# Optimization experiments

Measured on AMD Instinct MI355X. Metric: run time of the kernel, lower is better.

Reference implementation:

```python
import jax, jax.numpy as jnp
import numpy as np

N = 100000          # nodes
E = 1600000         # random edges (self loops appended in reference)
F_IN = 256          # dataset.num_features
NUM_CLASSES = 7     # dataset.num_classes
H = 2 * NUM_CLASSES # heads = 14
C = NUM_CLASSES     # per-head channels (concat=False)
NEG_SLOPE = 0.2     # GATConv default leaky_relu slope


def setup_inputs() -> dict:
    key = jax.random.key(0)
    ks = jax.random.split(key, 10)
    x = jax.random.normal(ks[0], (N, F_IN), jnp.float32)
    edge_index = jax.random.randint(ks[1], (2, E), 0, N, jnp.int32)
    def glorot(k, shape, fan_in):
        return jax.random.normal(k, shape, jnp.float32) * (1.0 / np.sqrt(fan_in))
    return {
        "x": x,
        "edge_index": edge_index,
        "W1": glorot(ks[2], (F_IN, H * C), F_IN),
        "a_src1": glorot(ks[3], (H, C), C),
        "a_dst1": glorot(ks[4], (H, C), C),
        "b1": jnp.zeros((C,), jnp.float32),
        "W2": glorot(ks[5], (C, H * C), C),
        "a_src2": glorot(ks[6], (H, C), C),
        "a_dst2": glorot(ks[7], (H, C), C),
        "b2": jnp.zeros((C,), jnp.float32),
    }


def gat_conv(x, src, dst, W, a_src, a_dst, b):
    # x: [N, Fin] -> per-head projections [N, H, C]
    xh = (x @ W).reshape(N, H, C)
    # per-node attention logits [N, H]
    al_src = jnp.einsum("nhc,hc->nh", xh, a_src)
    al_dst = jnp.einsum("nhc,hc->nh", xh, a_dst)
    # per-edge logits (message flows src -> dst)
    alpha = jax.nn.leaky_relu(al_src[src] + al_dst[dst], NEG_SLOPE)  # [E', H]
    # segment softmax over incoming edges of each destination node
    amax = jax.ops.segment_max(jax.lax.stop_gradient(alpha), dst, num_segments=N)
    alpha = jnp.exp(alpha - amax[dst])
    denom = jax.ops.segment_sum(alpha, dst, num_segments=N)
    alpha = alpha / denom[dst]
    # weighted messages, then MAX aggregation per destination (aggr='max')
    msg = alpha[:, :, None] * xh[src]                    # [E', H, C]
    out = jax.ops.segment_max(msg, dst, num_segments=N)  # [N, H, C]
    # concat=False -> mean over heads, plus bias
    return out.mean(axis=1) + b                          # [N, C]


def reference(x, edge_index, W1, a_src1, a_dst1, b1, W2, a_src2, a_dst2, b2):
    # GATConv(add_self_loops=True): append self loops so every node has >=1 in-edge
    loops = jnp.arange(N, dtype=edge_index.dtype)
    src = jnp.concatenate([edge_index[0], loops])
    dst = jnp.concatenate([edge_index[1], loops])
    h = gat_conv(x, src, dst, W1, a_src1, a_dst1, b1)
    h = jax.nn.relu(h)
    h = gat_conv(h, src, dst, W2, a_src2, a_dst2, b2)
    return jax.nn.log_softmax(h, axis=1)
```

## Files before the change

kernel.cpp:

```cpp
#include <hip/hip_runtime.h>
#include <math.h>

#define H  14
#define C  7
#define HC 98
#define FIN 256
#define NEG_SLOPE 0.2f
#define LOG2E 1.44269504088896f

#define BSHIFT 9
#define BSIZE  512
#define NBUCK_MAX 256

typedef __attribute__((ext_vector_type(8))) short short8;
typedef __attribute__((ext_vector_type(4))) float floatx4;
typedef _Float16 h2 __attribute__((ext_vector_type(2)));

#define WT_ROWS   112
#define WT_STRIDE 264
#define XA_STRIDE 40
#define VS_STRIDE 99

__device__ __forceinline__ unsigned bf16r(float f) {
    unsigned u = __float_as_uint(f);
    return (u + 0x7FFFu + ((u >> 16) & 1u)) >> 16;
}

__device__ __forceinline__ h2 u2h(unsigned u) { return __builtin_bit_cast(h2, u); }
__device__ __forceinline__ unsigned hpk(float a, float b) {
    h2 v = { (_Float16)a, (_Float16)b };
    return __builtin_bit_cast(unsigned, v);
}
__device__ __forceinline__ float hhi(unsigned w) {
    unsigned short s = (unsigned short)(w >> 16);
    return (float)__builtin_bit_cast(_Float16, s);
}
__device__ __forceinline__ h2 hshfl_max(h2 v, int mask) {
    int u = __builtin_bit_cast(int, v);
    int o = __shfl_xor(u, mask, 64);
    return __builtin_elementwise_max(v, u2h((unsigned)o));
}


__global__ void k_zero(int* __restrict__ p, int n) {
    int i = blockIdx.x * blockDim.x + threadIdx.x;
    if (i < n) p[i] = 0;
}

__global__ __launch_bounds__(256) void k_hist(const int* __restrict__ ei, int E,
                                              int* __restrict__ gcnt, int nb) {
    __shared__ int hist[NBUCK_MAX];
    const int t = threadIdx.x;
    for (int i = t; i < nb; i += 256) hist[i] = 0;
    __syncthreads();
    const int stride = gridDim.x * 256;
    for (int e = blockIdx.x * 256 + t; e < E; e += stride)
        atomicAdd(&hist[ei[E + e] >> BSHIFT], 1);
    __syncthreads();
    for (int i = t; i < nb; i += 256)
        if (hist[i]) atomicAdd(gcnt + i, hist[i]);
}

__global__ __launch_bounds__(1024) void k_bscan(const int* __restrict__ gcnt,
                                                int* __restrict__ boff, int* __restrict__ bcur,
                                                int* __restrict__ row_ptr, int nb, int N) {
    __shared__ int sd[1024];
    int t = threadIdx.x;
    int own = (t < nb) ? gcnt[t] : 0;
    sd[t] = own;
    __syncthreads();
    #pragma unroll
    for (int off = 1; off < 1024; off <<= 1) {
        int v = (t >= off) ? sd[t - off] : 0;
        __syncthreads();
        sd[t] += v;
        __syncthreads();
    }
    if (t < nb) {
        boff[t + 1] = sd[t];
        bcur[t] = sd[t] - own;
        if (t == nb - 1) row_ptr[N] = sd[t];
    }
    if (t == 0) boff[0] = 0;
}

__global__ __launch_bounds__(256) void k_part(const int* __restrict__ ei, int E,
                                              int* __restrict__ bcur, int2* __restrict__ pedge,
                                              int nb) {
    __shared__ int hist[NBUCK_MAX];
    __shared__ int start[NBUCK_MAX];
    const int t = threadIdx.x;
    const int chunk = (E + gridDim.x - 1) / gridDim.x;
    const int c0 = blockIdx.x * chunk;
    const int c1 = min(c0 + chunk, E);
    for (int i = t; i < nb; i += 256) hist[i] = 0;
    __syncthreads();
    for (int e = c0 + t; e < c1; e += 256)
        atomicAdd(&hist[ei[E + e] >> BSHIFT], 1);
    __syncthreads();
    for (int i = t; i < nb; i += 256) {
        int h = hist[i];
        start[i] = h ? atomicAdd(bcur + i, h) : 0;
        hist[i] = 0;
    }
    __syncthreads();
    for (int e = c0 + t; e < c1; e += 256) {
        int s = ei[e], d = ei[E + e];
        int b = d >> BSHIFT;
        int pos = start[b] + atomicAdd(&hist[b], 1);
        pedge[pos] = make_int2(s, d);
    }
}

__global__ __launch_bounds__(512) void k_bcsr(const int2* __restrict__ pedge,
                                              const int* __restrict__ boff,
                                              int* __restrict__ row_ptr, int* __restrict__ col,
                                              int N) {
    __shared__ int cnt[BSIZE];
    __shared__ int sc[BSIZE];
    __shared__ int cur[BSIZE];
    const int b  = blockIdx.x;
    const int t  = threadIdx.x;
    const int e0 = boff[b], e1 = boff[b + 1];
    const int base = b << BSHIFT;
    const int nv = min(BSIZE, N - base);
    cnt[t] = 0;
    __syncthreads();
    for (int e = e0 + t; e < e1; e += 512)
        atomicAdd(&cnt[pedge[e].y - base], 1);
    __syncthreads();
    sc[t] = cnt[t];
    __syncthreads();
    #pragma unroll
    for (int off = 1; off < BSIZE; off <<= 1) {
        int v = (t >= off) ? sc[t - off] : 0;
        __syncthreads();
        sc[t] += v;
        __syncthreads();
    }
    if (t < nv) {
        int excl = sc[t] - cnt[t];
        row_ptr[base + t] = e0 + excl;
        cur[t] = excl;
    }
    __syncthreads();
    for (int e = e0 + t; e < e1; e += 512) {
        int2 r = pedge[e];
        int d = r.y - base;
        int pos = e0 + atomicAdd(&cur[d], 1);
        col[pos] = r.x;
    }
}


__global__ void k_convW(const float* __restrict__ W, unsigned short* __restrict__ WtG) {
    int id = blockIdx.x * blockDim.x + threadIdx.x;
    int n = id >> 8, k = id & 255;
    float v = (n < HC) ? W[k * HC + n] : 0.f;
    WtG[id] = (unsigned short)(__float_as_uint(v) >> 16);
}

__global__ __launch_bounds__(256) void k_proj1_mfma(
    const float* __restrict__ x, const unsigned short* __restrict__ WtG,
    const float* __restrict__ asrc, const float* __restrict__ adst,
    uint4* __restrict__ xpack, float* __restrict__ aldst, int N)
{
    __shared__ unsigned short wt_s[WT_ROWS * WT_STRIDE];
    __shared__ unsigned short xa_s[64 * XA_STRIDE];
    __shared__ float as_s[HC], ad_s[HC];
    float* vals_s = (float*)wt_s;
    const int t  = threadIdx.x;
    const int wv = t >> 6;
    const int l  = t & 63;
    const int ln = l & 15;
    const int qd = l >> 4;
    const int rowBase = blockIdx.x * 64;

    #pragma unroll
    for (int i = 0; i < 14; ++i) {
        int f = i * 256 + t;
        int r = f >> 5, pos = f & 31;
        *(uint4*)(wt_s + r * WT_STRIDE + pos * 8) = ((const uint4*)WtG)[f];
    }
    if (t < HC) { as_s[t] = asrc[t]; ad_s[t] = adst[t]; }

    floatx4 acc[7] = {};

    for (int step = 0; step < 8; ++step) {
        const int k0 = step * 32;
        __syncthreads();
        #pragma unroll
        for (int i = 0; i < 2; ++i) {
            int idx = i * 256 + t;
            int r = idx >> 3, c4 = idx & 7;
            int gr = rowBase + r; if (gr >= N) gr = N - 1;
            float4 v = *(const float4*)(x + (size_t)gr * FIN + k0 + c4 * 4);
            ushort4 u;
            u.x = (unsigned short)(__float_as_uint(v.x) >> 16);
            u.y = (unsigned short)(__float_as_uint(v.y) >> 16);
            u.z = (unsigned short)(__float_as_uint(v.z) >> 16);
            u.w = (unsigned short)(__float_as_uint(v.w) >> 16);
            *(ushort4*)(xa_s + r * XA_STRIDE + c4 * 4) = u;
        }
        __syncthreads();
        short8 a = *(const short8*)(xa_s + ((wv << 4) + ln) * XA_STRIDE + qd * 8);
        #pragma unroll
        for (int ct = 0; ct < 7; ++ct) {
            short8 b = *(const short8*)(wt_s + (ct * 16 + ln) * WT_STRIDE + k0 + qd * 8);
            acc[ct] = __builtin_amdgcn_mfma_f32_16x16x32_bf16(a, b, acc[ct], 0, 0, 0);
        }
    }

    __syncthreads();
    #pragma unroll
    for (int ct = 0; ct < 7; ++ct) {
        int colg = ct * 16 + ln;
        if (colg < HC) {
            #pragma unroll
            for (int r = 0; r < 4; ++r)
                vals_s[((wv << 4) + (qd << 2) + r) * VS_STRIDE + colg] = acc[ct][r];
        }
    }
    __syncthreads();

    for (int p = t; p < 64 * H; p += 256) {
        int nl = p / H, h = p - nl * H;
        int gn = rowBase + nl;
        if (gn >= N) break;
        const float* vp = vals_s + nl * VS_STRIDE + h * C;
        float v[C];
        float s1 = 0.f, s2 = 0.f;
        #pragma unroll
        for (int c2 = 0; c2 < C; ++c2) {
            float f = vp[c2];
            v[c2] = f;
            s1 = fmaf(f, as_s[h * C + c2], s1);
            s2 = fmaf(f, ad_s[h * C + c2], s2);
        }
        uint4 pk;
        pk.x = hpk(v[0], v[1]);
        pk.y = hpk(v[2], v[3]);
        pk.z = hpk(v[4], v[5]);
        pk.w = hpk(v[6], s1 * LOG2E);
        xpack[(size_t)gn * H + h] = pk;
        aldst[(size_t)gn * H + h] = s2 * LOG2E;
    }
}


__global__ __launch_bounds__(256) void k_proj2_pack(
    const float* __restrict__ h1, const float* __restrict__ W,
    const float* __restrict__ asrc, const float* __restrict__ adst,
    uint4* __restrict__ xpack, float* __restrict__ aldst, int N)
{
    __shared__ float Ws[C * HC];
    __shared__ float as_s[HC], ad_s[HC];
    const int t = threadIdx.x;
    for (int i = t; i < C * HC; i += 256) Ws[i] = W[i];
    if (t < HC) { as_s[t] = asrc[t]; ad_s[t] = adst[t]; }
    __syncthreads();
    int n = blockIdx.x * 256 + t;
    if (n >= N) return;
    float xr[C];
    #pragma unroll
    for (int c2 = 0; c2 < C; ++c2) xr[c2] = h1[(size_t)n * C + c2];
    #pragma unroll
    for (int h = 0; h < H; ++h) {
        float v[C], s1 = 0.f, s2 = 0.f;
        #pragma unroll
        for (int c2 = 0; c2 < C; ++c2) {
            float acc = 0.f;
            #pragma unroll
            for (int k = 0; k < C; ++k)
                acc = fmaf(xr[k], Ws[k * HC + h * C + c2], acc);
            v[c2] = acc;
            s1 = fmaf(acc, as_s[h * C + c2], s1);
            s2 = fmaf(acc, ad_s[h * C + c2], s2);
        }
        uint4 pk;
        pk.x = hpk(v[0], v[1]);
        pk.y = hpk(v[2], v[3]);
        pk.z = hpk(v[4], v[5]);
        pk.w = hpk(v[6], s1 * LOG2E);
        xpack[(size_t)n * H + h] = pk;
        aldst[(size_t)n * H + h] = s2 * LOG2E;
    }
}

#define AGG_STEP(DEN, REC)                                              \
    {                                                                   \
        float l = hhi((REC).w) + ld;                                    \
        float p = __builtin_amdgcn_exp2f(fmaxf(l, 0.2f * l) - K);       \
        DEN += p;                                                       \
        _Float16 ph = (_Float16)p;                                      \
        h2 p2 = { ph, ph };                                             \
        m0 = __builtin_elementwise_max(m0, p2 * u2h((REC).x));          \
        m1 = __builtin_elementwise_max(m1, p2 * u2h((REC).y));          \
        m2 = __builtin_elementwise_max(m2, p2 * u2h((REC).z));          \
        m3 = __builtin_elementwise_max(m3, p2 * u2h((REC).w));          \
    }

template<int LAYER>
__global__ __launch_bounds__(256) void k_agg(
    const int* __restrict__ row_ptr, const int* __restrict__ col,
    const uint4* __restrict__ xpack, const float* __restrict__ aldst,
    const float* __restrict__ bias,
    float* __restrict__ h1, float* __restrict__ out, int N)
{
    const int t    = threadIdx.x;
    const int lane = t & 63;
    const int e4   = lane >> 4;
    const int h    = lane & 15;
    const int n    = blockIdx.x * 4 + (t >> 6);
    const bool act = (h < H) && (n < N);

    float den = 0.f, den2 = 0.f;
    h2 m0 = u2h(0xFC00FC00u), m1 = m0, m2 = m0, m3 = m0;
    float ld = 0.f, K = 0.f;

    if (act) {
        const int e0  = row_ptr[n];
        const int deg = row_ptr[n + 1] - e0;
        ld = aldst[(size_t)n * H + h];
        float kb = ld + 2.0f * LOG2E;
        K = fmaxf(kb, 0.2f * kb);

        if (e4 == 0) {
            uint4 pk = xpack[(size_t)n * H + h];
            float l = hhi(pk.w) + ld;
            float p = __builtin_amdgcn_exp2f(fmaxf(l, 0.2f * l) - K);
            den = p;
            _Float16 ph = (_Float16)p;
            h2 p2 = { ph, ph };
            m0 = p2 * u2h(pk.x);
            m1 = p2 * u2h(pk.y);
            m2 = p2 * u2h(pk.z);
            m3 = p2 * u2h(pk.w);
        }

        if (deg > 0) {
            const int last = deg - 1;
            int i = e4;
            int c0 = col[e0 + min(i,      last)];
            int c1 = col[e0 + min(i + 4,  last)];
            uint4 r0 = xpack[(size_t)c0 * H + h];
            uint4 r1 = xpack[(size_t)c1 * H + h];
            c0 = col[e0 + min(i + 8,  last)];
            c1 = col[e0 + min(i + 12, last)];
            for (; i < deg; i += 8) {
                uint4 curA = r0, curB = r1;
                r0 = xpack[(size_t)c0 * H + h];
                r1 = xpack[(size_t)c1 * H + h];
                c0 = col[e0 + min(i + 16, last)];
                c1 = col[e0 + min(i + 20, last)];
                AGG_STEP(den,  curA);
                if (i + 4 < deg) AGG_STEP(den2, curB);
            }
        }
    }
    den += den2;

    den += __shfl_xor(den, 16, 64);
    den += __shfl_xor(den, 32, 64);
    m0 = hshfl_max(m0, 16); m0 = hshfl_max(m0, 32);
    m1 = hshfl_max(m1, 16); m1 = hshfl_max(m1, 32);
    m2 = hshfl_max(m2, 16); m2 = hshfl_max(m2, 32);
    m3 = hshfl_max(m3, 16); m3 = hshfl_max(m3, 32);

    float v[C];
    if (act) {
        float rd = 1.f / den;
        v[0] = (float)m0.x * rd; v[1] = (float)m0.y * rd;
        v[2] = (float)m1.x * rd; v[3] = (float)m1.y * rd;
        v[4] = (float)m2.x * rd; v[5] = (float)m2.y * rd;
        v[6] = (float)m3.x * rd;
    } else {
        #pragma unroll
        for (int c = 0; c < C; ++c) v[c] = 0.f;
    }

    #pragma unroll
    for (int off = 1; off <= 8; off <<= 1) {
        #pragma unroll
        for (int c = 0; c < C; ++c) v[c] += __shfl_xor(v[c], off, 64);
    }

    if (n >= N) return;
    if (LAYER == 1) {
        if (lane < C) {
            float myv = v[0];
            #pragma unroll
            for (int c = 1; c < C; ++c) if (lane == c) myv = v[c];
            h1[(size_t)n * C + lane] = fmaxf(myv * (1.f / H) + bias[lane], 0.f);
        }
    } else {
        float o[C];
        #pragma unroll
        for (int c = 0; c < C; ++c) o[c] = v[c] * (1.f / H) + bias[c];
        float mv = o[0];
        #pragma unroll
        for (int c = 1; c < C; ++c) mv = fmaxf(mv, o[c]);
        float lse = 0.f;
        #pragma unroll
        for (int c = 0; c < C; ++c) lse += __expf(o[c] - mv);
        lse = logf(lse);
        if (lane < C) {
            float myo = o[0];
            #pragma unroll
            for (int c = 1; c < C; ++c) if (lane == c) myo = o[c];
            out[(size_t)n * C + lane] = myo - mv - lse;
        }
    }
}


static inline size_t align16(size_t v) { return (v + 15) & ~(size_t)15; }

extern "C" void kernel_launch(void* const* d_in, const int* in_sizes, int n_in,
                              void* d_out, int out_size, void* d_ws, size_t ws_size,
                              hipStream_t stream)
{
    const float* x     = (const float*)d_in[0];
    const int*   ei    = (const int*)d_in[1];
    const float* W1    = (const float*)d_in[2];
    const float* asrc1 = (const float*)d_in[3];
    const float* adst1 = (const float*)d_in[4];
    const float* b1    = (const float*)d_in[5];
    const float* W2    = (const float*)d_in[6];
    const float* asrc2 = (const float*)d_in[7];
    const float* adst2 = (const float*)d_in[8];
    const float* b2    = (const float*)d_in[9];

    const int N  = in_sizes[0] / FIN;
    const int E  = in_sizes[1] / 2;
    const int nb = (N + BSIZE - 1) >> BSHIFT;

    char* w = (char*)d_ws;
    uint4* xpack   = (uint4*)w; w += align16((size_t)N * H * 16);
    int2*  pedge   = (int2*)w;  w += align16((size_t)E * 8);
    float* aldst   = (float*)w; w += align16((size_t)N * H * 4);
    float* h1      = (float*)w; w += align16((size_t)N * C * 4);
    int*   row_ptr = (int*)w;   w += align16((size_t)(N + 1) * 4);
    int*   col     = (int*)w;   w += align16((size_t)E * 4);
    int*   gcnt    = (int*)w;   w += align16((size_t)nb * 4);
    int*   boff    = (int*)w;   w += align16((size_t)(nb + 1) * 4);
    int*   bcur    = (int*)w;   w += align16((size_t)nb * 4);
    unsigned short* WtG = (unsigned short*)w; w += align16((size_t)WT_ROWS * FIN * 2);

    const int gAgg  = (N + 3) / 4;
    const int gMfma = (N + 63) / 64;
    const int g256N = (N + 255) / 256;

    k_zero<<<1, 256, 0, stream>>>(gcnt, nb);
    k_hist<<<256, 256, 0, stream>>>(ei, E, gcnt, nb);
    k_bscan<<<1, 1024, 0, stream>>>(gcnt, boff, bcur, row_ptr, nb, N);
    k_part<<<256, 256, 0, stream>>>(ei, E, bcur, pedge, nb);
    k_bcsr<<<nb, 512, 0, stream>>>(pedge, boff, row_ptr, col, N);

    k_convW<<<(WT_ROWS * FIN + 255) / 256, 256, 0, stream>>>(W1, WtG);
    k_proj1_mfma<<<gMfma, 256, 0, stream>>>(x, WtG, asrc1, adst1, xpack, aldst, N);
    k_agg<1><<<gAgg, 256, 0, stream>>>(row_ptr, col, xpack, aldst, b1,
                                       h1, (float*)d_out, N);
    k_proj2_pack<<<g256N, 256, 0, stream>>>(h1, W2, asrc2, adst2, xpack, aldst, N);
    k_agg<2><<<gAgg, 256, 0, stream>>>(row_ptr, col, xpack, aldst, b2,
                                       h1, (float*)d_out, N);
}
```

Measured before the change: 409.8 us.

## Split head aggregation into two passes over half-size packed feature planes

Packed per-node head records are reorganized into two planes of seven heads each, and each layer's aggregation runs as two kernels that each gather from only one plane. The first pass writes partial head sums to a scratch buffer, and the second adds them and applies bias plus ReLU or log-softmax. The goal is to shrink the randomly gathered working set so it stays resident in cache. The cost is reading the CSR twice, one more launch per layer, and an extra partial-sum round trip.

```diff
diff --git a/kernel.cpp b/kernel.cpp
--- a/kernel.cpp
+++ b/kernel.cpp
@@ -242,7 +242,9 @@
         pk.y = hpk(v[2], v[3]);
         pk.z = hpk(v[4], v[5]);
         pk.w = hpk(v[6], s1 * LOG2E);
-        xpack[(size_t)gn * H + h] = pk;
+        int pass = (h >= C) ? 1 : 0;
+        int slot = h - pass * C;
+        xpack[((size_t)pass * N + gn) * 8 + slot] = pk;
         aldst[(size_t)gn * H + h] = s2 * LOG2E;
     }
 }
@@ -282,7 +284,9 @@
         pk.y = hpk(v[2], v[3]);
         pk.z = hpk(v[4], v[5]);
         pk.w = hpk(v[6], s1 * LOG2E);
-        xpack[(size_t)n * H + h] = pk;
+        int pass = (h >= C) ? 1 : 0;
+        int slot = h - pass * C;
+        xpack[((size_t)pass * N + n) * 8 + slot] = pk;
         aldst[(size_t)n * H + h] = s2 * LOG2E;
     }
 }
@@ -300,19 +304,20 @@
         m3 = __builtin_elementwise_max(m3, p2 * u2h((REC).w));          \
     }
 
-template<int LAYER>
-__global__ __launch_bounds__(256) void k_agg(
+template<int LAYER, int PASS>
+__global__ __launch_bounds__(256) void k_agg7(
     const int* __restrict__ row_ptr, const int* __restrict__ col,
-    const uint4* __restrict__ xpack, const float* __restrict__ aldst,
-    const float* __restrict__ bias,
+    const uint4* __restrict__ xp,
+    const float* __restrict__ aldst, const float* __restrict__ bias,
+    float* __restrict__ psum,
     float* __restrict__ h1, float* __restrict__ out, int N)
 {
     const int t    = threadIdx.x;
     const int lane = t & 63;
-    const int e4   = lane >> 4;
-    const int h    = lane & 15;
+    const int e8   = lane >> 3;
+    const int h7   = lane & 7;
     const int n    = blockIdx.x * 4 + (t >> 6);
-    const bool act = (h < H) && (n < N);
+    const bool act = (h7 < C) && (n < N);
 
     float den = 0.f, den2 = 0.f;
     h2 m0 = u2h(0xFC00FC00u), m1 = m0, m2 = m0, m3 = m0;
@@ -321,12 +326,12 @@
     if (act) {
         const int e0  = row_ptr[n];
         const int deg = row_ptr[n + 1] - e0;
-        ld = aldst[(size_t)n * H + h];
+        ld = aldst[(size_t)n * H + PASS * C + h7];
         float kb = ld + 2.0f * LOG2E;
         K = fmaxf(kb, 0.2f * kb);
 
-        if (e4 == 0) {
-            uint4 pk = xpack[(size_t)n * H + h];
+        if (e8 == 0) {
+            uint4 pk = xp[(size_t)n * 8 + h7];
             float l = hhi(pk.w) + ld;
             float p = __builtin_amdgcn_exp2f(fmaxf(l, 0.2f * l) - K);
             den = p;
@@ -340,32 +345,33 @@
 
         if (deg > 0) {
             const int last = deg - 1;
-            int i = e4;
+            int i = e8;
             int c0 = col[e0 + min(i,      last)];
-            int c1 = col[e0 + min(i + 4,  last)];
-            uint4 r0 = xpack[(size_t)c0 * H + h];
-            uint4 r1 = xpack[(size_t)c1 * H + h];
-            c0 = col[e0 + min(i + 8,  last)];
-            c1 = col[e0 + min(i + 12, last)];
-            for (; i < deg; i += 8) {
+            int c1 = col[e0 + min(i + 8,  last)];
+            uint4 r0 = xp[(size_t)c0 * 8 + h7];
+            uint4 r1 = xp[(size_t)c1 * 8 + h7];
+            c0 = col[e0 + min(i + 16, last)];
+            c1 = col[e0 + min(i + 24, last)];
+            for (; i < deg; i += 16) {
                 uint4 curA = r0, curB = r1;
-                r0 = xpack[(size_t)c0 * H + h];
-                r1 = xpack[(size_t)c1 * H + h];
-                c0 = col[e0 + min(i + 16, last)];
-                c1 = col[e0 + min(i + 20, last)];
+                r0 = xp[(size_t)c0 * 8 + h7];
+                r1 = xp[(size_t)c1 * 8 + h7];
+                c0 = col[e0 + min(i + 32, last)];
+                c1 = col[e0 + min(i + 40, last)];
                 AGG_STEP(den,  curA);
-                if (i + 4 < deg) AGG_STEP(den2, curB);
+                if (i + 8 < deg) AGG_STEP(den2, curB);
             }
         }
     }
     den += den2;
 
+    den += __shfl_xor(den, 8, 64);
     den += __shfl_xor(den, 16, 64);
     den += __shfl_xor(den, 32, 64);
-    m0 = hshfl_max(m0, 16); m0 = hshfl_max(m0, 32);
-    m1 = hshfl_max(m1, 16); m1 = hshfl_max(m1, 32);
-    m2 = hshfl_max(m2, 16); m2 = hshfl_max(m2, 32);
-    m3 = hshfl_max(m3, 16); m3 = hshfl_max(m3, 32);
+    m0 = hshfl_max(m0, 8); m0 = hshfl_max(m0, 16); m0 = hshfl_max(m0, 32);
+    m1 = hshfl_max(m1, 8); m1 = hshfl_max(m1, 16); m1 = hshfl_max(m1, 32);
+    m2 = hshfl_max(m2, 8); m2 = hshfl_max(m2, 16); m2 = hshfl_max(m2, 32);
+    m3 = hshfl_max(m3, 8); m3 = hshfl_max(m3, 16); m3 = hshfl_max(m3, 32);
 
     float v[C];
     if (act) {
@@ -380,35 +386,46 @@
     }
 
     #pragma unroll
-    for (int off = 1; off <= 8; off <<= 1) {
+    for (int off = 1; off <= 4; off <<= 1) {
         #pragma unroll
         for (int c = 0; c < C; ++c) v[c] += __shfl_xor(v[c], off, 64);
     }
 
     if (n >= N) return;
-    if (LAYER == 1) {
+
+    if (PASS == 0) {
         if (lane < C) {
             float myv = v[0];
             #pragma unroll
             for (int c = 1; c < C; ++c) if (lane == c) myv = v[c];
-            h1[(size_t)n * C + lane] = fmaxf(myv * (1.f / H) + bias[lane], 0.f);
+            psum[(size_t)n * 8 + lane] = myv;
         }
     } else {
         float o[C];
         #pragma unroll
-        for (int c = 0; c < C; ++c) o[c] = v[c] * (1.f / H) + bias[c];
-        float mv = o[0];
-        #pragma unroll
-        for (int c = 1; c < C; ++c) mv = fmaxf(mv, o[c]);
-        float lse = 0.f;
-        #pragma unroll
-        for (int c = 0; c < C; ++c) lse += __expf(o[c] - mv);
-        lse = logf(lse);
-        if (lane < C) {
-            float myo = o[0];
+        for (int c = 0; c < C; ++c)
+            o[c] = (v[c] + psum[(size_t)n * 8 + c]) * (1.f / H) + bias[c];
+        if (LAYER == 1) {
+            if (lane < C) {
+                float myo = o[0];
+                #pragma unroll
+                for (int c = 1; c < C; ++c) if (lane == c) myo = o[c];
+                h1[(size_t)n * C + lane] = fmaxf(myo, 0.f);
+            }
+        } else {
+            float mv = o[0];
             #pragma unroll
-            for (int c = 1; c < C; ++c) if (lane == c) myo = o[c];
-            out[(size_t)n * C + lane] = myo - mv - lse;
+            for (int c = 1; c < C; ++c) mv = fmaxf(mv, o[c]);
+            float lse = 0.f;
+            #pragma unroll
+            for (int c = 0; c < C; ++c) lse += __expf(o[c] - mv);
+            lse = logf(lse);
+            if (lane < C) {
+                float myo = o[0];
+                #pragma unroll
+                for (int c = 1; c < C; ++c) if (lane == c) myo = o[c];
+                out[(size_t)n * C + lane] = myo - mv - lse;
+            }
         }
     }
 }
@@ -436,7 +453,7 @@
     const int nb = (N + BSIZE - 1) >> BSHIFT;
 
     char* w = (char*)d_ws;
-    uint4* xpack   = (uint4*)w; w += align16((size_t)N * H * 16);
+    uint4* xpack   = (uint4*)w; w += align16((size_t)N * 16 * 16);
     int2*  pedge   = (int2*)w;  w += align16((size_t)E * 8);
     float* aldst   = (float*)w; w += align16((size_t)N * H * 4);
     float* h1      = (float*)w; w += align16((size_t)N * C * 4);
@@ -447,6 +464,10 @@
     int*   bcur    = (int*)w;   w += align16((size_t)nb * 4);
     unsigned short* WtG = (unsigned short*)w; w += align16((size_t)WT_ROWS * FIN * 2);
 
+    float* psum = (float*)pedge;
+    const uint4* xpA = xpack;
+    const uint4* xpB = xpack + (size_t)N * 8;
+
     const int gAgg  = (N + 3) / 4;
     const int gMfma = (N + 63) / 64;
     const int g256N = (N + 255) / 256;
@@ -459,9 +480,13 @@
 
     k_convW<<<(WT_ROWS * FIN + 255) / 256, 256, 0, stream>>>(W1, WtG);
     k_proj1_mfma<<<gMfma, 256, 0, stream>>>(x, WtG, asrc1, adst1, xpack, aldst, N);
-    k_agg<1><<<gAgg, 256, 0, stream>>>(row_ptr, col, xpack, aldst, b1,
-                                       h1, (float*)d_out, N);
+    k_agg7<1, 0><<<gAgg, 256, 0, stream>>>(row_ptr, col, xpA, aldst, b1, psum,
+                                           h1, (float*)d_out, N);
+    k_agg7<1, 1><<<gAgg, 256, 0, stream>>>(row_ptr, col, xpB, aldst, b1, psum,
+                                           h1, (float*)d_out, N);
     k_proj2_pack<<<g256N, 256, 0, stream>>>(h1, W2, asrc2, adst2, xpack, aldst, N);
-    k_agg<2><<<gAgg, 256, 0, stream>>>(row_ptr, col, xpack, aldst, b2,
-                                       h1, (float*)d_out, N);
-}
+    k_agg7<2, 0><<<gAgg, 256, 0, stream>>>(row_ptr, col, xpA, aldst, b2, psum,
+                                           h1, (float*)d_out, N);
+    k_agg7<2, 1><<<gAgg, 256, 0, stream>>>(row_ptr, col, xpB, aldst, b2, psum,
+                                           h1, (float*)d_out, N);
+}
```

Result: slower. 489.4 us (+19.4%).
